# Kernel optimization log

Hardware: AMD Instinct MI355X
Metric: run time of the kernel (lower is better)

The kernel has to match this reference:

```python
import jax, jax.numpy as jnp
import numpy as np

L, H, Wn, C = 2048, 768, 1024, 64


def setup_inputs() -> dict:
    key = jax.random.key(0)
    ks = jax.random.split(key, 12)
    s = 1.0 / np.sqrt(H)
    s3 = 1.0 / np.sqrt(3 * H)
    return {
        "tok_embs": jax.random.normal(ks[0], (L, H), jnp.float32),
        "wmask": jax.random.randint(ks[1], (L,), 0, Wn + 1),  # 1-indexed word positions, 0 = ignore
        "text_length": Wn,
        "label_embs": jax.random.normal(ks[2], (C, H), jnp.float32),
        "W_tok": jax.random.normal(ks[3], (H, 2 * H), jnp.float32) * s,
        "b_tok": jnp.zeros((2 * H,), jnp.float32),
        "W_lab": jax.random.normal(ks[4], (H, 2 * H), jnp.float32) * s,
        "b_lab": jnp.zeros((2 * H,), jnp.float32),
        "W1": jax.random.normal(ks[5], (3 * H, H), jnp.float32) * s3,
        "b1": jnp.zeros((H,), jnp.float32),
        "W2": jax.random.normal(ks[6], (H, 3), jnp.float32) * s,
        "b2": jnp.zeros((3,), jnp.float32),
    }


def reference(tok_embs, wmask, text_length, label_embs, W_tok, b_tok, W_lab, b_lab, W1, b1, W2, b2):
    Wd = text_length
    Hd = tok_embs.shape[-1]
    # --- word-level scatter pooling: we[wmask-1] = tok_embs where wmask > 0 ---
    # route masked-out tokens to a dummy row Wd, then drop it (jit-safe, no nonzero)
    tgt = jnp.where(wmask > 0, wmask - 1, Wd)
    we = jnp.zeros((Wd + 1, Hd), tok_embs.dtype).at[tgt].set(tok_embs)[:Wd]  # (W, H)
    # --- scorer ---
    t = (we @ W_tok + b_tok).reshape(Wd, 2, Hd)        # (W, 2, H)
    lb = (label_embs @ W_lab + b_lab).reshape(-1, 2, Hd)  # (C, 2, H)
    Cd = lb.shape[0]
    t0 = jnp.broadcast_to(t[:, None, 0, :], (Wd, Cd, Hd))
    l0 = jnp.broadcast_to(lb[None, :, 0, :], (Wd, Cd, Hd))
    prod = t[:, None, 1, :] * lb[None, :, 1, :]        # (W, C, H)
    cat = jnp.concatenate([t0, l0, prod], axis=-1)     # (W, C, 3H)
    h = jax.nn.relu(cat @ W1 + b1)                     # (W, C, H)
    scores = h @ W2 + b2                               # (W, C, 3)
    return scores
```

## Files before the change

### kernel.cpp

```cpp
#include <hip/hip_runtime.h>
#include <hip/hip_bf16.h>

static constexpr int Hd = 768;
static constexpr int H2 = 1536;
static constexpr int Cn = 64;

typedef __attribute__((ext_vector_type(8))) short short8;
typedef __attribute__((ext_vector_type(8))) _Float16 half8;
typedef __attribute__((ext_vector_type(4))) float f32x4;
typedef unsigned short us;

__device__ inline void split1(float x, us& h, us& l) {
    __hip_bfloat16 hb = __float2bfloat16(x);
    float hf = __bfloat162float(hb);
    __hip_bfloat16 lb_ = __float2bfloat16(x - hf);
    h = *reinterpret_cast<us*>(&hb);
    l = *reinterpret_cast<us*>(&lb_);
}

__device__ inline us f2b(float x) {
    __hip_bfloat16 b = __float2bfloat16(x);
    return *reinterpret_cast<us*>(&b);
}

__device__ inline us f2h(float x) {
    _Float16 h = (_Float16)x;
    return *reinterpret_cast<us*>(&h);
}

__device__ inline short8 hmul8(short8 a, short8 b) {
    half8 x = __builtin_bit_cast(half8, a);
    half8 y = __builtin_bit_cast(half8, b);
    half8 r = x * y;
    return __builtin_bit_cast(short8, r);
}

__device__ inline void gload16(const void* g, void* l) {
    __builtin_amdgcn_global_load_lds(
        (const __attribute__((address_space(1))) unsigned int*)g,
        (__attribute__((address_space(3))) unsigned int*)l, 16, 0, 0);
}

__global__ void k_init(int* widx, int Wd) {
    int i = blockIdx.x * 256 + threadIdx.x;
    if (i < Wd) widx[i] = -1;
}

__global__ void k_scatter(const int* __restrict__ wmask, int* widx, int L, int Wd) {
    int i = blockIdx.x * 256 + threadIdx.x;
    if (i < L) {
        int m = wmask[i];
        if (m > 0 && m <= Wd) atomicMax(&widx[m - 1], i);
    }
}

__global__ void k_build_we_split(const float4* __restrict__ tok, const int* __restrict__ widx,
                                 us* __restrict__ weh, us* __restrict__ wel, int Wd) {
    int i = blockIdx.x * 256 + threadIdx.x;
    if (i >= Wd * 192) return;
    int w = i / 192, c4 = i - w * 192;
    int idx = widx[w];
    float4 v = (idx >= 0) ? tok[idx * 192 + c4] : float4{0.f, 0.f, 0.f, 0.f};
    us hh[4], ll[4];
    split1(v.x, hh[0], ll[0]);
    split1(v.y, hh[1], ll[1]);
    split1(v.z, hh[2], ll[2]);
    split1(v.w, hh[3], ll[3]);
    size_t o = (size_t)w * Hd + c4 * 4;
    *(ushort4*)&weh[o] = ushort4{hh[0], hh[1], hh[2], hh[3]};
    *(ushort4*)&wel[o] = ushort4{ll[0], ll[1], ll[2], ll[3]};
}

struct TSArgs {
    const float* src[5];
    us* th[5];
    us* tl[5];
    int ld[5];
    int N[5];
    int fmt[5];
};
__global__ __launch_bounds__(256)
void k_tsplit(TSArgs a) {
    __shared__ float tile[64][65];
    const int z = blockIdx.z;
    const int n0 = blockIdx.x * 64, k0 = blockIdx.y * 64;
    if (n0 >= a.N[z]) return;
    const float* W = a.src[z];
    const int ld = a.ld[z];
    for (int idx = threadIdx.x; idx < 4096; idx += 256) {
        int kk = idx >> 6, nn = idx & 63;
        tile[kk][nn] = W[(size_t)(k0 + kk) * ld + n0 + nn];
    }
    __syncthreads();
    us* Th = a.th[z];
    us* Tl = a.tl[z];
    const int fmt = a.fmt[z];
    for (int idx = threadIdx.x; idx < 4096; idx += 256) {
        int nn = idx >> 6, kk = idx & 63;
        size_t o = (size_t)(n0 + nn) * Hd + k0 + kk;
        if (fmt) {
            Th[o] = f2h(tile[kk][nn]);
        } else {
            us h, l;
            split1(tile[kk][nn], h, l);
            Th[o] = h;
            Tl[o] = l;
        }
    }
}

__global__ __launch_bounds__(256)
void k_split(const float* __restrict__ x, int lda, int cols,
             us* __restrict__ h, us* __restrict__ l, int n4) {
    int i = blockIdx.x * 256 + threadIdx.x;
    if (i >= n4) return;
    int c4 = cols >> 2;
    int row = i / c4, cc = (i - row * c4) * 4;
    float4 v = *(const float4*)&x[(size_t)row * lda + cc];
    us hh[4], ll[4];
    split1(v.x, hh[0], ll[0]);
    split1(v.y, hh[1], ll[1]);
    split1(v.z, hh[2], ll[2]);
    split1(v.w, hh[3], ll[3]);
    size_t o = (size_t)row * cols + cc;
    *(ushort4*)&h[o] = ushort4{hh[0], hh[1], hh[2], hh[3]};
    *(ushort4*)&l[o] = ushort4{ll[0], ll[1], ll[2], ll[3]};
}

__global__ __launch_bounds__(256)
void k_gemm2(const us* __restrict__ Ah, const us* __restrict__ Al,
             const us* __restrict__ BhT, const us* __restrict__ BlT,
             float* __restrict__ Cpart, int M, int N, int K) {
    __shared__ __align__(16) us S[2][4][64 * 32];
    const int tid = threadIdx.x, wave = tid >> 6, lane = tid & 63;
    const int quad = lane >> 4, l15 = lane & 15;
    const int wm = wave & 1, wn = wave >> 1;
    const int m0 = blockIdx.y * 64, n0 = blockIdx.x * 64;
    const int Ks = K / gridDim.z, kbeg = blockIdx.z * Ks, kend = kbeg + Ks;
    float* C = Cpart + (size_t)blockIdx.z * M * N;

    const int srow = wave * 16 + (lane >> 2), soff = (lane & 3) * 8;
    const size_t gaB = (size_t)(m0 + srow) * K + soff;
    const size_t gbB = (size_t)(n0 + srow) * K + soff;
    const int lo = wave * 16 * 32;

    f32x4 acc[2][2];
#pragma unroll
    for (int a = 0; a < 2; ++a)
#pragma unroll
        for (int b = 0; b < 2; ++b) acc[a][b] = (f32x4){0.f, 0.f, 0.f, 0.f};

    auto stage = [&](int p, int k0) {
        gload16(Ah + gaB + k0, &S[p][0][lo]);
        gload16(Al + gaB + k0, &S[p][1][lo]);
        gload16(BhT + gbB + k0, &S[p][2][lo]);
        gload16(BlT + gbB + k0, &S[p][3][lo]);
    };

    int p = 0;
    stage(0, kbeg);
    for (int k0 = kbeg; k0 < kend; k0 += 32) {
        __syncthreads();
        if (k0 + 32 < kend) stage(p ^ 1, k0 + 32);
        short8 ah[2], al[2], bh[2], bl[2];
#pragma unroll
        for (int mt = 0; mt < 2; ++mt) {
            int off = (wm * 32 + mt * 16 + l15) * 32 + quad * 8;
            ah[mt] = *(const short8*)&S[p][0][off];
            al[mt] = *(const short8*)&S[p][1][off];
        }
#pragma unroll
        for (int nt = 0; nt < 2; ++nt) {
            int off = (wn * 32 + nt * 16 + l15) * 32 + quad * 8;
            bh[nt] = *(const short8*)&S[p][2][off];
            bl[nt] = *(const short8*)&S[p][3][off];
        }
#pragma unroll
        for (int mt = 0; mt < 2; ++mt)
#pragma unroll
            for (int nt = 0; nt < 2; ++nt) {
                acc[mt][nt] = __builtin_amdgcn_mfma_f32_16x16x32_bf16(al[mt], bh[nt], acc[mt][nt], 0, 0, 0);
                acc[mt][nt] = __builtin_amdgcn_mfma_f32_16x16x32_bf16(ah[mt], bl[nt], acc[mt][nt], 0, 0, 0);
                acc[mt][nt] = __builtin_amdgcn_mfma_f32_16x16x32_bf16(ah[mt], bh[nt], acc[mt][nt], 0, 0, 0);
            }
        p ^= 1;
    }
#pragma unroll
    for (int mt = 0; mt < 2; ++mt)
#pragma unroll
        for (int nt = 0; nt < 2; ++nt) {
            int col = n0 + wn * 32 + nt * 16 + l15;
#pragma unroll
            for (int reg = 0; reg < 4; ++reg) {
                int row = m0 + wm * 32 + mt * 16 + quad * 4 + reg;
                C[(size_t)row * N + col] = acc[mt][nt][reg];
            }
        }
}

__global__ __launch_bounds__(256)
void k_gemm3(const us* __restrict__ Ah, const us* __restrict__ Al,
             const us* __restrict__ BhT, const us* __restrict__ BlT,
             const float* __restrict__ bias, float* __restrict__ outF,
             us* __restrict__ sh, us* __restrict__ sl, us* __restrict__ bh16,
             int fp16out, int scols, int N, int K) {
    __shared__ __align__(16) us S[2][4][64 * 32];
    const int tid = threadIdx.x, wave = tid >> 6, lane = tid & 63;
    const int quad = lane >> 4, l15 = lane & 15;
    const int wm = wave & 1, wn = wave >> 1;
    const int m0 = blockIdx.y * 64, n0 = blockIdx.x * 64;

    const int srow = wave * 16 + (lane >> 2), soff = (lane & 3) * 8;
    const size_t gaB = (size_t)(m0 + srow) * K + soff;
    const size_t gbB = (size_t)(n0 + srow) * K + soff;
    const int lo = wave * 16 * 32;

    f32x4 acc[2][2];
#pragma unroll
    for (int a = 0; a < 2; ++a)
#pragma unroll
        for (int b = 0; b < 2; ++b) acc[a][b] = (f32x4){0.f, 0.f, 0.f, 0.f};

    auto stage = [&](int p, int k0) {
        gload16(Ah + gaB + k0, &S[p][0][lo]);
        gload16(Al + gaB + k0, &S[p][1][lo]);
        gload16(BhT + gbB + k0, &S[p][2][lo]);
        gload16(BlT + gbB + k0, &S[p][3][lo]);
    };

    int p = 0;
    stage(0, 0);
    for (int k0 = 0; k0 < K; k0 += 32) {
        __syncthreads();
        if (k0 + 32 < K) stage(p ^ 1, k0 + 32);
        short8 ah[2], al[2], bh[2], bl[2];
#pragma unroll
        for (int mt = 0; mt < 2; ++mt) {
            int off = (wm * 32 + mt * 16 + l15) * 32 + quad * 8;
            ah[mt] = *(const short8*)&S[p][0][off];
            al[mt] = *(const short8*)&S[p][1][off];
        }
#pragma unroll
        for (int nt = 0; nt < 2; ++nt) {
            int off = (wn * 32 + nt * 16 + l15) * 32 + quad * 8;
            bh[nt] = *(const short8*)&S[p][2][off];
            bl[nt] = *(const short8*)&S[p][3][off];
        }
#pragma unroll
        for (int mt = 0; mt < 2; ++mt)
#pragma unroll
            for (int nt = 0; nt < 2; ++nt) {
                acc[mt][nt] = __builtin_amdgcn_mfma_f32_16x16x32_bf16(al[mt], bh[nt], acc[mt][nt], 0, 0, 0);
                acc[mt][nt] = __builtin_amdgcn_mfma_f32_16x16x32_bf16(ah[mt], bl[nt], acc[mt][nt], 0, 0, 0);
                acc[mt][nt] = __builtin_amdgcn_mfma_f32_16x16x32_bf16(ah[mt], bh[nt], acc[mt][nt], 0, 0, 0);
            }
        p ^= 1;
    }
#pragma unroll
    for (int mt = 0; mt < 2; ++mt)
#pragma unroll
        for (int nt = 0; nt < 2; ++nt) {
            int col = n0 + wn * 32 + nt * 16 + l15;
            float bb = bias ? bias[col] : 0.f;
#pragma unroll
            for (int reg = 0; reg < 4; ++reg) {
                int row = m0 + wm * 32 + mt * 16 + quad * 4 + reg;
                float v = acc[mt][nt][reg] + bb;
                if (outF) outF[(size_t)row * N + col] = v;
                if (sh) {
                    if (col < scols) {
                        us h, l;
                        split1(v, h, l);
                        size_t o = (size_t)row * scols + col;
                        sh[o] = h;
                        sl[o] = l;
                    } else if (bh16) {
                        bh16[(size_t)row * scols + (col - scols)] = fp16out ? f2h(v) : f2b(v);
                    }
                }
            }
        }
}

__global__ __launch_bounds__(256)
void k_reduce(const float* __restrict__ part, int S, int MN, int N,
              const float* __restrict__ bias, float* __restrict__ outF,
              us* __restrict__ sh, us* __restrict__ sl, int scols,
              us* __restrict__ bh16, int fp16out) {
    int i = blockIdx.x * 256 + threadIdx.x;
    if (i >= MN) return;
    float v = 0.f;
    for (int s = 0; s < S; ++s) v += part[(size_t)s * MN + i];
    int row = i / N, col = i - row * N;
    if (bias) v += bias[col];
    if (outF) outF[i] = v;
    if (col < scols) {
        if (sh) {
            us h, l;
            split1(v, h, l);
            size_t o = (size_t)row * scols + col;
            sh[o] = h;
            sl[o] = l;
        }
    } else if (bh16) {
        bh16[(size_t)row * scols + (col - scols)] = fp16out ? f2h(v) : f2b(v);
    }
}

__global__ __launch_bounds__(512, 1)
void k_mfma13(const us* __restrict__ t1b,
              const us* __restrict__ W1ct,
              const us* __restrict__ lb1b,
              const float* __restrict__ Aw,
              const float* __restrict__ Bc,
              const float* __restrict__ W2,
              float* __restrict__ scr) {
    __shared__ __align__(16) us RA[3][8192];
    __shared__ __align__(16) us RB[3][8192];
    __shared__ __align__(16) us lbs[Hd];
    __shared__ float sred[256 * 3];

    const int tid = threadIdx.x, wave = tid >> 6, lane = tid & 63;
    const int quad = lane >> 4, l15 = lane & 15;
    const int wm2 = wave >> 2, wn4 = wave & 3;

    const int b = blockIdx.x;
    const int xcd = b & 7, s5 = b >> 3;
    const int cl = s5 & 7, idx = s5 >> 3;
    const int jb = idx % 3, wb = idx / 3;
    const int c  = xcd * 8 + cl;

    for (int i = tid; i < 256 * 3; i += 512) sred[i] = 0.f;
    if (tid < 96) *(short8*)&lbs[tid * 8] = *(const short8*)&lb1b[(size_t)c * Hd + tid * 8];

    const int q = wave & 3, rh = wave >> 2;
    const us* gA0 = W1ct + (size_t)(jb * 256 + (rh * 2 + 0) * 64 + lane) * Hd + q * 8;
    const us* gA1 = W1ct + (size_t)(jb * 256 + (rh * 2 + 1) * 64 + lane) * Hd + q * 8;
    const us* gB0 = t1b + (size_t)(wb * 256 + (rh * 2 + 0) * 64 + lane) * Hd + q * 8;
    const us* gB1 = t1b + (size_t)(wb * 256 + (rh * 2 + 1) * 64 + lane) * Hd + q * 8;
    const int dA0 = q * 2048 + (rh * 2 + 0) * 512;
    const int dA1 = q * 2048 + (rh * 2 + 1) * 512;

    f32x4 acc[8][4];
#pragma unroll
    for (int mf = 0; mf < 8; ++mf)
#pragma unroll
        for (int nf = 0; nf < 4; ++nf) acc[mf][nf] = (f32x4){0.f, 0.f, 0.f, 0.f};

    auto stagePh = [&](int slot, int k0, int j) {
        if (j == 0) { gload16(gA0 + k0, &RA[slot][dA0]); gload16(gB0 + k0, &RB[slot][dA0]); }
        else        { gload16(gA1 + k0, &RA[slot][dA1]); gload16(gB1 + k0, &RB[slot][dA1]); }
    };

    const int rbA = quad * 2048 + (wm2 * 128 + l15) * 8;
    const int rbB = quad * 2048 + (wn4 * 64 + l15) * 8;

    __syncthreads();

    stagePh(0, 0, 0);  stagePh(0, 0, 1);
    stagePh(1, 32, 0); stagePh(1, 32, 1);

#pragma unroll
    for (int s = 0; s < 24; ++s) {
        const int slot = s % 3;
        if (s < 23) asm volatile("s_waitcnt vmcnt(4)" ::: "memory");
        else        asm volatile("s_waitcnt vmcnt(0)" ::: "memory");
        __builtin_amdgcn_s_barrier();
        __builtin_amdgcn_sched_barrier(0);
        short8 bF[4], aF[4];
        short8 lv = *(const short8*)&lbs[s * 32 + quad * 8];
#pragma unroll
        for (int nf = 0; nf < 4; ++nf) bF[nf] = *(const short8*)&RB[slot][rbB + nf * 128];
#pragma unroll
        for (int i = 0; i < 4; ++i) aF[i] = *(const short8*)&RA[slot][rbA + i * 128];
        if (s + 2 < 24) stagePh((s + 2) % 3, (s + 2) * 32, 0);
        asm volatile("s_waitcnt lgkmcnt(0)" ::: "memory");
        __builtin_amdgcn_sched_barrier(0);
        __builtin_amdgcn_s_setprio(1);
#pragma unroll
        for (int i = 0; i < 4; ++i) {
            short8 aS = hmul8(aF[i], lv);
#pragma unroll
            for (int nf = 0; nf < 4; ++nf)
                acc[i][nf] = __builtin_amdgcn_mfma_f32_16x16x32_f16(
                    __builtin_bit_cast(half8, aS),
                    __builtin_bit_cast(half8, bF[nf]), acc[i][nf], 0, 0, 0);
        }
        __builtin_amdgcn_s_setprio(0);
        __builtin_amdgcn_s_barrier();
#pragma unroll
        for (int i = 0; i < 4; ++i) aF[i] = *(const short8*)&RA[slot][rbA + (4 + i) * 128];
        if (s + 2 < 24) stagePh((s + 2) % 3, (s + 2) * 32, 1);
        asm volatile("s_waitcnt lgkmcnt(0)" ::: "memory");
        __builtin_amdgcn_sched_barrier(0);
        __builtin_amdgcn_s_setprio(1);
#pragma unroll
        for (int i = 0; i < 4; ++i) {
            short8 aS = hmul8(aF[i], lv);
#pragma unroll
            for (int nf = 0; nf < 4; ++nf)
                acc[4 + i][nf] = __builtin_amdgcn_mfma_f32_16x16x32_f16(
                    __builtin_bit_cast(half8, aS),
                    __builtin_bit_cast(half8, bF[nf]), acc[4 + i][nf], 0, 0, 0);
        }
        __builtin_amdgcn_s_setprio(0);
    }

    float sv[4][3];
#pragma unroll
    for (int nf = 0; nf < 4; ++nf)
#pragma unroll
        for (int r = 0; r < 3; ++r) sv[nf][r] = 0.f;

#pragma unroll
    for (int mf = 0; mf < 8; ++mf) {
        const int jg = jb * 256 + wm2 * 128 + mf * 16 + quad * 4;
        float4 bc4 = *(const float4*)&Bc[(size_t)c * Hd + jg];
        float bcv[4] = {bc4.x, bc4.y, bc4.z, bc4.w};
        float w2v[4][3];
#pragma unroll
        for (int reg = 0; reg < 4; ++reg)
#pragma unroll
            for (int r = 0; r < 3; ++r) w2v[reg][r] = W2[(jg + reg) * 3 + r];
#pragma unroll
        for (int nf = 0; nf < 4; ++nf) {
            const int w = wb * 256 + wn4 * 64 + nf * 16 + l15;
            float4 a4 = *(const float4*)&Aw[(size_t)w * Hd + jg];
            float av[4] = {a4.x, a4.y, a4.z, a4.w};
#pragma unroll
            for (int reg = 0; reg < 4; ++reg) {
                float h = acc[mf][nf][reg] + av[reg] + bcv[reg];
                h = h > 0.f ? h : 0.f;
                sv[nf][0] += h * w2v[reg][0];
                sv[nf][1] += h * w2v[reg][1];
                sv[nf][2] += h * w2v[reg][2];
            }
        }
    }
#pragma unroll
    for (int nf = 0; nf < 4; ++nf) {
#pragma unroll
        for (int r = 0; r < 3; ++r) {
            float s = sv[nf][r];
            s += __shfl_xor(s, 16);
            s += __shfl_xor(s, 32);
            sv[nf][r] = s;
        }
        if (quad == 0) {
            const int wl = wn4 * 64 + nf * 16 + l15;
            atomicAdd(&sred[wl * 3 + 0], sv[nf][0]);
            atomicAdd(&sred[wl * 3 + 1], sv[nf][1]);
            atomicAdd(&sred[wl * 3 + 2], sv[nf][2]);
        }
    }
    __syncthreads();

    float* slab = scr + (size_t)jb * (1024 * Cn * 3);
    for (int i = tid; i < 256 * 3; i += 512) {
        int wl = i / 3, r = i - wl * 3;
        slab[((size_t)(wb * 256 + wl) * Cn + c) * 3 + r] = sred[i];
    }
}

__global__ __launch_bounds__(256)
void k_scores(const float* __restrict__ scr, const float* __restrict__ b2,
              float* __restrict__ out, int n) {
    int i = blockIdx.x * 256 + threadIdx.x;
    if (i >= n) return;
    float v = b2[i % 3];
#pragma unroll
    for (int s = 0; s < 3; ++s) v += scr[(size_t)s * n + i];
    out[i] = v;
}

extern "C" void kernel_launch(void* const* d_in, const int* in_sizes, int n_in,
                              void* d_out, int out_size, void* d_ws, size_t ws_size,
                              hipStream_t stream) {
    const float* tok    = (const float*)d_in[0];
    const int*   wmask  = (const int*)d_in[1];
    const float* labe   = (const float*)d_in[3];
    const float* W_tok  = (const float*)d_in[4];
    const float* b_tok  = (const float*)d_in[5];
    const float* W_lab  = (const float*)d_in[6];
    const float* b_lab  = (const float*)d_in[7];
    const float* W1     = (const float*)d_in[8];
    const float* b1     = (const float*)d_in[9];
    const float* W2     = (const float*)d_in[10];
    const float* b2     = (const float*)d_in[11];
    float* out = (float*)d_out;

    const int L  = in_sizes[1];
    const int Wd = out_size / (Cn * 3);

    char* ws = (char*)d_ws;
    size_t off = 0;
    auto alloc = [&](size_t bytes) { char* p = ws + off; off += (bytes + 255) & ~(size_t)255; return p; };
    int*   widx  = (int*)alloc(4096);
    float* Abuf  = (float*)alloc((size_t)Wd * Hd * 4);
    float* Bbuf  = (float*)alloc((size_t)Cn * Hd * 4);
    us* W1ct  = (us*)alloc((size_t)Hd * Hd * 2);
    us* W1cl  = (us*)alloc((size_t)Hd * Hd * 2);
    us* t1b   = (us*)alloc((size_t)Wd * Hd * 2);
    us* lb1b  = (us*)alloc((size_t)Cn * Hd * 2);
    float* scr = (float*)alloc((size_t)3 * Wd * Cn * 3 * 4);
    us* WtTh  = (us*)alloc((size_t)H2 * Hd * 2);
    us* WtTl  = (us*)alloc((size_t)H2 * Hd * 2);
    us* WlTh  = (us*)alloc((size_t)H2 * Hd * 2);
    us* WlTl  = (us*)alloc((size_t)H2 * Hd * 2);
    us* W1aTh = (us*)alloc((size_t)Hd * Hd * 2);
    us* W1aTl = (us*)alloc((size_t)Hd * Hd * 2);
    us* W1bTh = (us*)alloc((size_t)Hd * Hd * 2);
    us* W1bTl = (us*)alloc((size_t)Hd * Hd * 2);
    us* weh   = (us*)alloc((size_t)Wd * Hd * 2);
    us* wel   = (us*)alloc((size_t)Wd * Hd * 2);
    us* lah   = (us*)alloc((size_t)Cn * Hd * 2);
    us* lal   = (us*)alloc((size_t)Cn * Hd * 2);
    us* t0h   = (us*)alloc((size_t)Wd * Hd * 2);
    us* t0l   = (us*)alloc((size_t)Wd * Hd * 2);
    us* lb0h  = (us*)alloc((size_t)Cn * Hd * 2);
    us* lb0l  = (us*)alloc((size_t)Cn * Hd * 2);
    float* part = (float*)alloc((size_t)8 * Cn * H2 * 4);

    k_init<<<(Wd + 255) / 256, 256, 0, stream>>>(widx, Wd);
    k_scatter<<<(L + 255) / 256, 256, 0, stream>>>(wmask, widx, L, Wd);
    k_build_we_split<<<(Wd * 192 + 255) / 256, 256, 0, stream>>>((const float4*)tok, widx, weh, wel, Wd);

    TSArgs ts;
    ts.src[0] = W_tok;  ts.th[0] = WtTh;  ts.tl[0] = WtTl;  ts.ld[0] = H2; ts.N[0] = H2; ts.fmt[0] = 0;
    ts.src[1] = W_lab;  ts.th[1] = WlTh;  ts.tl[1] = WlTl;  ts.ld[1] = H2; ts.N[1] = H2; ts.fmt[1] = 0;
    ts.src[2] = W1;                         ts.th[2] = W1aTh; ts.tl[2] = W1aTl; ts.ld[2] = Hd; ts.N[2] = Hd; ts.fmt[2] = 0;
    ts.src[3] = W1 + (size_t)Hd * Hd;       ts.th[3] = W1bTh; ts.tl[3] = W1bTl; ts.ld[3] = Hd; ts.N[3] = Hd; ts.fmt[3] = 0;
    ts.src[4] = W1 + (size_t)2 * Hd * Hd;   ts.th[4] = W1ct;  ts.tl[4] = W1cl;  ts.ld[4] = Hd; ts.N[4] = Hd; ts.fmt[4] = 1;
    k_tsplit<<<dim3(H2 / 64, Hd / 64, 5), 256, 0, stream>>>(ts);

    k_split<<<(Cn * Hd / 4 + 255) / 256, 256, 0, stream>>>(labe, Hd, Hd, lah, lal, Cn * Hd / 4);

    k_gemm3<<<dim3(H2 / 64, Wd / 64), 256, 0, stream>>>(weh, wel, WtTh, WtTl, b_tok,
                                                        nullptr, t0h, t0l, t1b, 1, Hd, H2, Hd);

    k_gemm2<<<dim3(H2 / 64, 1, 8), 256, 0, stream>>>(lah, lal, WlTh, WlTl, part, Cn, H2, Hd);
    k_reduce<<<(Cn * H2 + 255) / 256, 256, 0, stream>>>(part, 8, Cn * H2, H2, b_lab, nullptr, lb0h, lb0l, Hd, lb1b, 1);

    k_gemm3<<<dim3(Hd / 64, Wd / 64), 256, 0, stream>>>(t0h, t0l, W1aTh, W1aTl, nullptr,
                                                        Abuf, nullptr, nullptr, nullptr, 0, 0, Hd, Hd);

    k_gemm2<<<dim3(Hd / 64, 1, 8), 256, 0, stream>>>(lb0h, lb0l, W1bTh, W1bTl, part, Cn, Hd, Hd);
    k_reduce<<<(Cn * Hd + 255) / 256, 256, 0, stream>>>(part, 8, Cn * Hd, Hd, b1, Bbuf, nullptr, nullptr, Hd, nullptr, 0);

    k_mfma13<<<768, 512, 0, stream>>>(t1b, W1ct, lb1b, Abuf, Bbuf, W2, scr);

    k_scores<<<(Wd * Cn * 3 + 255) / 256, 256, 0, stream>>>(scr, b2, out, Wd * Cn * 3);
}
```

Measured before the change: 308.8 us.

## Retile scorer MFMA kernel to 128x128 tiles over two labels with two blocks per CU

The fused product-GEMM kernel now has each block compute a 128-word by 128-hidden tile for two labels at once, with each wave group handling one label. Before, a block did a 256x256 tile for a single label. The smaller LDS footprint and launch_bounds(512,2) allow two blocks per CU, and the grid doubles to 1536 blocks. Because the hidden dimension is split into six partial-score slabs instead of three, the final scores kernel has more reduction traffic and the scratch buffer is larger. Each fetched W1/t1 tile is reused across two labels, but tiles are smaller, so per-tile operand reuse drops. Global reload traffic may therefore rise.

```diff
diff --git a/kernel.cpp b/kernel.cpp
--- a/kernel.cpp
+++ b/kernel.cpp
@@ -307,158 +307,149 @@
     }
 }
 
-__global__ __launch_bounds__(512, 1)
-void k_mfma13(const us* __restrict__ t1b,
+__global__ __launch_bounds__(512, 2)
+void k_mfma14(const us* __restrict__ t1b,
               const us* __restrict__ W1ct,
               const us* __restrict__ lb1b,
               const float* __restrict__ Aw,
               const float* __restrict__ Bc,
               const float* __restrict__ W2,
               float* __restrict__ scr) {
-    __shared__ __align__(16) us RA[3][8192];
-    __shared__ __align__(16) us RB[3][8192];
-    __shared__ __align__(16) us lbs[Hd];
-    __shared__ float sred[256 * 3];
+    __shared__ __align__(16) us RA[3][4096];
+    __shared__ __align__(16) us RB[3][4096];
+    __shared__ __align__(16) us lbs[2][Hd];
+    __shared__ float sred[2 * 128 * 3];
 
     const int tid = threadIdx.x, wave = tid >> 6, lane = tid & 63;
     const int quad = lane >> 4, l15 = lane & 15;
-    const int wm2 = wave >> 2, wn4 = wave & 3;
+    const int jm = wave & 1, wn = (wave >> 1) & 1, cw = wave >> 2;
 
     const int b = blockIdx.x;
-    const int xcd = b & 7, s5 = b >> 3;
-    const int cl = s5 & 7, idx = s5 >> 3;
-    const int jb = idx % 3, wb = idx / 3;
-    const int c  = xcd * 8 + cl;
-
-    for (int i = tid; i < 256 * 3; i += 512) sred[i] = 0.f;
-    if (tid < 96) *(short8*)&lbs[tid * 8] = *(const short8*)&lb1b[(size_t)c * Hd + tid * 8];
-
-    const int q = wave & 3, rh = wave >> 2;
-    const us* gA0 = W1ct + (size_t)(jb * 256 + (rh * 2 + 0) * 64 + lane) * Hd + q * 8;
-    const us* gA1 = W1ct + (size_t)(jb * 256 + (rh * 2 + 1) * 64 + lane) * Hd + q * 8;
-    const us* gB0 = t1b + (size_t)(wb * 256 + (rh * 2 + 0) * 64 + lane) * Hd + q * 8;
-    const us* gB1 = t1b + (size_t)(wb * 256 + (rh * 2 + 1) * 64 + lane) * Hd + q * 8;
-    const int dA0 = q * 2048 + (rh * 2 + 0) * 512;
-    const int dA1 = q * 2048 + (rh * 2 + 1) * 512;
-
-    f32x4 acc[8][4];
-#pragma unroll
-    for (int mf = 0; mf < 8; ++mf)
+    const int xcd = b & 7, slot5 = b >> 3;
+    const int jx = slot5 >> 5;
+    const int cp = slot5 & 31;
+    const int c0 = cp * 2;
+    const int jt = jx * 128, m0 = xcd * 128;
+
+    for (int i = tid; i < 2 * 128 * 3; i += 512) sred[i] = 0.f;
+    if (tid < 192) {
+        int cc = tid / 96, o = (tid - cc * 96) * 8;
+        *(short8*)&lbs[cc][o] = *(const short8*)&lb1b[(size_t)(c0 + cc) * Hd + o];
+    }
+
+    const int rhalf = wave & 1, qc = wave >> 1;
+    const us* gA = W1ct + (size_t)(jt + rhalf * 64 + lane) * Hd + qc * 8;
+    const us* gB = t1b + (size_t)(m0 + rhalf * 64 + lane) * Hd + qc * 8;
+    const int dst = wave * 512;
+
+    f32x4 acc[4][4];
+#pragma unroll
+    for (int mf = 0; mf < 4; ++mf)
 #pragma unroll
         for (int nf = 0; nf < 4; ++nf) acc[mf][nf] = (f32x4){0.f, 0.f, 0.f, 0.f};
 
-    auto stagePh = [&](int slot, int k0, int j) {
-        if (j == 0) { gload16(gA0 + k0, &RA[slot][dA0]); gload16(gB0 + k0, &RB[slot][dA0]); }
-        else        { gload16(gA1 + k0, &RA[slot][dA1]); gload16(gB1 + k0, &RB[slot][dA1]); }
-    };
-
-    const int rbA = quad * 2048 + (wm2 * 128 + l15) * 8;
-    const int rbB = quad * 2048 + (wn4 * 64 + l15) * 8;
+    const int rbA = quad * 1024 + (jm * 64 + l15) * 8;
+    const int rbB = quad * 1024 + (wn * 64 + l15) * 8;
 
     __syncthreads();
 
-    stagePh(0, 0, 0);  stagePh(0, 0, 1);
-    stagePh(1, 32, 0); stagePh(1, 32, 1);
+    gload16(gA + 0,  &RA[0][dst]);  gload16(gB + 0,  &RB[0][dst]);
+    gload16(gA + 32, &RA[1][dst]);  gload16(gB + 32, &RB[1][dst]);
 
 #pragma unroll
     for (int s = 0; s < 24; ++s) {
-        const int slot = s % 3;
-        if (s < 23) asm volatile("s_waitcnt vmcnt(4)" ::: "memory");
+        const int sl = s % 3;
+        if (s < 23) asm volatile("s_waitcnt vmcnt(2)" ::: "memory");
         else        asm volatile("s_waitcnt vmcnt(0)" ::: "memory");
         __builtin_amdgcn_s_barrier();
         __builtin_amdgcn_sched_barrier(0);
+        short8 lv = *(const short8*)&lbs[cw][s * 32 + quad * 8];
         short8 bF[4], aF[4];
-        short8 lv = *(const short8*)&lbs[s * 32 + quad * 8];
-#pragma unroll
-        for (int nf = 0; nf < 4; ++nf) bF[nf] = *(const short8*)&RB[slot][rbB + nf * 128];
-#pragma unroll
-        for (int i = 0; i < 4; ++i) aF[i] = *(const short8*)&RA[slot][rbA + i * 128];
-        if (s + 2 < 24) stagePh((s + 2) % 3, (s + 2) * 32, 0);
+#pragma unroll
+        for (int nf = 0; nf < 4; ++nf) bF[nf] = *(const short8*)&RB[sl][rbB + nf * 128];
+        aF[0] = *(const short8*)&RA[sl][rbA + 0 * 128];
+        aF[1] = *(const short8*)&RA[sl][rbA + 1 * 128];
+        if (s + 2 < 24) gload16(gA + (s + 2) * 32, &RA[(s + 2) % 3][dst]);
         asm volatile("s_waitcnt lgkmcnt(0)" ::: "memory");
         __builtin_amdgcn_sched_barrier(0);
         __builtin_amdgcn_s_setprio(1);
 #pragma unroll
-        for (int i = 0; i < 4; ++i) {
-            short8 aS = hmul8(aF[i], lv);
+        for (int mf = 0; mf < 2; ++mf) {
+            short8 aS = hmul8(aF[mf], lv);
 #pragma unroll
             for (int nf = 0; nf < 4; ++nf)
-                acc[i][nf] = __builtin_amdgcn_mfma_f32_16x16x32_f16(
+                acc[mf][nf] = __builtin_amdgcn_mfma_f32_16x16x32_f16(
                     __builtin_bit_cast(half8, aS),
-                    __builtin_bit_cast(half8, bF[nf]), acc[i][nf], 0, 0, 0);
+                    __builtin_bit_cast(half8, bF[nf]), acc[mf][nf], 0, 0, 0);
         }
         __builtin_amdgcn_s_setprio(0);
         __builtin_amdgcn_s_barrier();
-#pragma unroll
-        for (int i = 0; i < 4; ++i) aF[i] = *(const short8*)&RA[slot][rbA + (4 + i) * 128];
-        if (s + 2 < 24) stagePh((s + 2) % 3, (s + 2) * 32, 1);
+        aF[2] = *(const short8*)&RA[sl][rbA + 2 * 128];
+        aF[3] = *(const short8*)&RA[sl][rbA + 3 * 128];
+        if (s + 2 < 24) gload16(gB + (s + 2) * 32, &RB[(s + 2) % 3][dst]);
         asm volatile("s_waitcnt lgkmcnt(0)" ::: "memory");
         __builtin_amdgcn_sched_barrier(0);
         __builtin_amdgcn_s_setprio(1);
 #pragma unroll
-        for (int i = 0; i < 4; ++i) {
-            short8 aS = hmul8(aF[i], lv);
+        for (int mf = 2; mf < 4; ++mf) {
+            short8 aS = hmul8(aF[mf], lv);
 #pragma unroll
             for (int nf = 0; nf < 4; ++nf)
-                acc[4 + i][nf] = __builtin_amdgcn_mfma_f32_16x16x32_f16(
+                acc[mf][nf] = __builtin_amdgcn_mfma_f32_16x16x32_f16(
                     __builtin_bit_cast(half8, aS),
-                    __builtin_bit_cast(half8, bF[nf]), acc[4 + i][nf], 0, 0, 0);
+                    __builtin_bit_cast(half8, bF[nf]), acc[mf][nf], 0, 0, 0);
         }
         __builtin_amdgcn_s_setprio(0);
     }
 
-    float sv[4][3];
-#pragma unroll
-    for (int nf = 0; nf < 4; ++nf)
-#pragma unroll
-        for (int r = 0; r < 3; ++r) sv[nf][r] = 0.f;
-
-#pragma unroll
-    for (int mf = 0; mf < 8; ++mf) {
-        const int jg = jb * 256 + wm2 * 128 + mf * 16 + quad * 4;
-        float4 bc4 = *(const float4*)&Bc[(size_t)c * Hd + jg];
-        float bcv[4] = {bc4.x, bc4.y, bc4.z, bc4.w};
-        float w2v[4][3];
+    const int cme = c0 + cw;
+    float bcv[4][4], w2v[4][4][3];
+#pragma unroll
+    for (int mf = 0; mf < 4; ++mf) {
+        const int jg = jt + jm * 64 + mf * 16 + quad * 4;
+        float4 b4 = *(const float4*)&Bc[(size_t)cme * Hd + jg];
+        bcv[mf][0] = b4.x; bcv[mf][1] = b4.y; bcv[mf][2] = b4.z; bcv[mf][3] = b4.w;
 #pragma unroll
         for (int reg = 0; reg < 4; ++reg)
 #pragma unroll
-            for (int r = 0; r < 3; ++r) w2v[reg][r] = W2[(jg + reg) * 3 + r];
-#pragma unroll
-        for (int nf = 0; nf < 4; ++nf) {
-            const int w = wb * 256 + wn4 * 64 + nf * 16 + l15;
-            float4 a4 = *(const float4*)&Aw[(size_t)w * Hd + jg];
+            for (int r = 0; r < 3; ++r) w2v[mf][reg][r] = W2[(jg + reg) * 3 + r];
+    }
+
+#pragma unroll
+    for (int nf = 0; nf < 4; ++nf) {
+        const int w = m0 + wn * 64 + nf * 16 + l15;
+        const float* awp = Aw + (size_t)w * Hd + jt + jm * 64;
+        float s0 = 0.f, s1 = 0.f, s2 = 0.f;
+#pragma unroll
+        for (int mf = 0; mf < 4; ++mf) {
+            float4 a4 = *(const float4*)&awp[mf * 16 + quad * 4];
             float av[4] = {a4.x, a4.y, a4.z, a4.w};
 #pragma unroll
             for (int reg = 0; reg < 4; ++reg) {
-                float h = acc[mf][nf][reg] + av[reg] + bcv[reg];
+                float h = acc[mf][nf][reg] + av[reg] + bcv[mf][reg];
                 h = h > 0.f ? h : 0.f;
-                sv[nf][0] += h * w2v[reg][0];
-                sv[nf][1] += h * w2v[reg][1];
-                sv[nf][2] += h * w2v[reg][2];
+                s0 += h * w2v[mf][reg][0];
+                s1 += h * w2v[mf][reg][1];
+                s2 += h * w2v[mf][reg][2];
             }
         }
-    }
-#pragma unroll
-    for (int nf = 0; nf < 4; ++nf) {
-#pragma unroll
-        for (int r = 0; r < 3; ++r) {
-            float s = sv[nf][r];
-            s += __shfl_xor(s, 16);
-            s += __shfl_xor(s, 32);
-            sv[nf][r] = s;
-        }
+        s0 += __shfl_xor(s0, 16); s0 += __shfl_xor(s0, 32);
+        s1 += __shfl_xor(s1, 16); s1 += __shfl_xor(s1, 32);
+        s2 += __shfl_xor(s2, 16); s2 += __shfl_xor(s2, 32);
         if (quad == 0) {
-            const int wl = wn4 * 64 + nf * 16 + l15;
-            atomicAdd(&sred[wl * 3 + 0], sv[nf][0]);
-            atomicAdd(&sred[wl * 3 + 1], sv[nf][1]);
-            atomicAdd(&sred[wl * 3 + 2], sv[nf][2]);
+            const int wl = wn * 64 + nf * 16 + l15;
+            atomicAdd(&sred[cw * 384 + wl * 3 + 0], s0);
+            atomicAdd(&sred[cw * 384 + wl * 3 + 1], s1);
+            atomicAdd(&sred[cw * 384 + wl * 3 + 2], s2);
         }
     }
     __syncthreads();
 
-    float* slab = scr + (size_t)jb * (1024 * Cn * 3);
-    for (int i = tid; i < 256 * 3; i += 512) {
-        int wl = i / 3, r = i - wl * 3;
-        slab[((size_t)(wb * 256 + wl) * Cn + c) * 3 + r] = sred[i];
+    float* slab = scr + ((size_t)jx * 1024 * Cn + (size_t)m0 * Cn) * 3;
+    for (int i = tid; i < 2 * 128 * 3; i += 512) {
+        int cc = i / 384, j = i - cc * 384;
+        int wl = j / 3, r = j - wl * 3;
+        slab[((size_t)wl * Cn + (c0 + cc)) * 3 + r] = sred[i];
     }
 }
 
@@ -469,7 +460,7 @@
     if (i >= n) return;
     float v = b2[i % 3];
 #pragma unroll
-    for (int s = 0; s < 3; ++s) v += scr[(size_t)s * n + i];
+    for (int s = 0; s < 6; ++s) v += scr[(size_t)s * n + i];
     out[i] = v;
 }
 
@@ -502,7 +493,7 @@
     us* W1cl  = (us*)alloc((size_t)Hd * Hd * 2);
     us* t1b   = (us*)alloc((size_t)Wd * Hd * 2);
     us* lb1b  = (us*)alloc((size_t)Cn * Hd * 2);
-    float* scr = (float*)alloc((size_t)3 * Wd * Cn * 3 * 4);
+    float* scr = (float*)alloc((size_t)6 * Wd * Cn * 3 * 4);
     us* WtTh  = (us*)alloc((size_t)H2 * Hd * 2);
     us* WtTl  = (us*)alloc((size_t)H2 * Hd * 2);
     us* WlTh  = (us*)alloc((size_t)H2 * Hd * 2);
@@ -547,7 +538,7 @@
     k_gemm2<<<dim3(Hd / 64, 1, 8), 256, 0, stream>>>(lb0h, lb0l, W1bTh, W1bTl, part, Cn, Hd, Hd);
     k_reduce<<<(Cn * Hd + 255) / 256, 256, 0, stream>>>(part, 8, Cn * Hd, Hd, b1, Bbuf, nullptr, nullptr, Hd, nullptr, 0);
 
-    k_mfma13<<<768, 512, 0, stream>>>(t1b, W1ct, lb1b, Abuf, Bbuf, W2, scr);
+    k_mfma14<<<1536, 512, 0, stream>>>(t1b, W1ct, lb1b, Abuf, Bbuf, W2, scr);
 
     k_scores<<<(Wd * Cn * 3 + 255) / 256, 256, 0, stream>>>(scr, b2, out, Wd * Cn * 3);
 }
```

Result: faster. 293.1 us (-5.1%).
